# Optimization experiments

Hardware: AMD Instinct MI355X
Metric: run time of the kernel (lower is better)

Reference implementation:

```python
import jax, jax.numpy as jnp
import numpy as np

B, N, F, F1 = 1024, 75, 512, 256
NEG = -1.0e9
ALPHA = 0.2  # LeakyReLU slope


def setup_inputs() -> dict:
    key = jax.random.key(0)
    k1, k2, k3, k4 = jax.random.split(key, 4)
    X = jax.random.normal(k1, (B, N, F), dtype=jnp.float32)
    A = jax.random.randint(k2, (N, N), 0, 2, dtype=jnp.int32)  # binary adjacency
    W = jax.random.normal(k3, (F, F1), dtype=jnp.float32) * (1.0 / np.sqrt(F))
    a = jax.random.normal(k4, (2, F1, 1), dtype=jnp.float32) * (1.0 / np.sqrt(F1))
    return {"X": X, "A": A, "W": W, "a": a}


def reference(X, A, W, a):
    # Linear projection: [B, N, F1]
    h = jnp.einsum('bnf,fo->bno', X, W)
    # Additive attention logits
    att_self = jnp.einsum('bno,od->bnd', h, a[0])        # [B, N, 1]
    att_neigh = jnp.einsum('bno,od->bnd', h, a[1])       # [B, N, 1]
    e = att_self + jnp.swapaxes(att_neigh, 1, 2)         # [B, N, N]
    e = jax.nn.leaky_relu(e, ALPHA)
    # Adjacency mask: disallowed edges get large negative bias
    adj = A.astype(h.dtype)                               # [N, N]
    e = e + NEG * (1.0 - adj)[None, :, :]
    # Normalize over neighbors, aggregate
    alpha = jax.nn.softmax(e, axis=-1)                    # [B, N, N]
    out = jnp.einsum('bij,bjo->bio', alpha, h)            # [B, N, F1]
    return jnp.concatenate([out, h], axis=-1)             # [B, N, 2*F1]
```

## Files before the change

kernel.cpp:

```cpp
#include <hip/hip_runtime.h>
#include <hip/hip_bf16.h>
#include <math.h>

typedef __bf16 bf16_t;
typedef __bf16 bf16x4_t __attribute__((ext_vector_type(4)));
typedef __bf16 bf16x8 __attribute__((ext_vector_type(8)));
typedef float f32x4 __attribute__((ext_vector_type(4)));
typedef unsigned long long u64;

#define NB 1024
#define NN 75
#define KF 512
#define F1 256
#define HSTR 100
#define ASTR 100

__global__ __launch_bounds__(256) void wt_kernel(const float* __restrict__ W,
                                                 bf16_t* __restrict__ Wt) {
    __shared__ float tile[64][65];
    const int kb = blockIdx.x * 64;
    const int nb = blockIdx.y * 64;
    const int tc = threadIdx.x & 63;
    const int tr = threadIdx.x >> 6;
#pragma unroll
    for (int r = tr; r < 64; r += 4)
        tile[r][tc] = W[(size_t)(kb + r) * F1 + nb + tc];
    __syncthreads();
#pragma unroll
    for (int r = tr; r < 64; r += 4)
        Wt[(size_t)(nb + r) * KF + kb + tc] = (bf16_t)tile[tc][r];
}

__global__ __launch_bounds__(256) void gemm_kernel(const float* __restrict__ X,
                                                   const bf16_t* __restrict__ Wt,
                                                   float* __restrict__ out) {
    __shared__ __align__(16) bf16_t Xb[2 * 2048];

    const int t = threadIdx.x;
    const int w = t >> 6;
    const int l = t & 63;
    const int lc = l & 15;
    const int lr = l >> 4;
    const int m0 = blockIdx.x * 64;

    const int xrow  = ((t >> 6) << 4) + (t & 15);
    const int kpart = ((t >> 4) & 3) * 8;
    const float* xsrc = X + (size_t)(m0 + xrow) * KF + kpart;

    const bf16_t* wp0 = Wt + (size_t)(w * 64 + 0 * 16 + lc) * KF + lr * 8;
    const bf16_t* wp1 = Wt + (size_t)(w * 64 + 1 * 16 + lc) * KF + lr * 8;
    const bf16_t* wp2 = Wt + (size_t)(w * 64 + 2 * 16 + lc) * KF + lr * 8;
    const bf16_t* wp3 = Wt + (size_t)(w * 64 + 3 * 16 + lc) * KF + lr * 8;

    f32x4 acc[4][4];
#pragma unroll
    for (int i = 0; i < 4; ++i)
#pragma unroll
        for (int j = 0; j < 4; ++j) acc[i][j] = (f32x4){0.f, 0.f, 0.f, 0.f};

    float4 xa, xb;
    bf16x8 wA[4], wB[4];

#define WLOAD(WREG, KS)                                        \
    WREG[0] = *(const bf16x8*)(wp0 + (KS) * 32);               \
    WREG[1] = *(const bf16x8*)(wp1 + (KS) * 32);               \
    WREG[2] = *(const bf16x8*)(wp2 + (KS) * 32);               \
    WREG[3] = *(const bf16x8*)(wp3 + (KS) * 32);

#define GSTEP(KS, WREG)                                                        \
    {                                                                          \
        const bf16_t* Xc = Xb + ((KS) & 1) * 2048;                             \
        bf16x8 af[4];                                                          \
        _Pragma("unroll")                                                      \
        for (int mt = 0; mt < 4; ++mt)                                         \
            af[mt] = *(const bf16x8*)&Xc[(mt * 64 + l) * 8];                   \
        _Pragma("unroll")                                                      \
        for (int mt = 0; mt < 4; ++mt)                                         \
            _Pragma("unroll")                                                  \
            for (int ntl = 0; ntl < 4; ++ntl)                                  \
                acc[mt][ntl] = __builtin_amdgcn_mfma_f32_16x16x32_bf16(        \
                    af[mt], WREG[ntl], acc[mt][ntl], 0, 0, 0);                 \
        if ((KS) < 15) {                                                       \
            bf16x8 v;                                                          \
            v[0]=(bf16_t)xa.x; v[1]=(bf16_t)xa.y;                              \
            v[2]=(bf16_t)xa.z; v[3]=(bf16_t)xa.w;                              \
            v[4]=(bf16_t)xb.x; v[5]=(bf16_t)xb.y;                              \
            v[6]=(bf16_t)xb.z; v[7]=(bf16_t)xb.w;                              \
            *(bf16x8*)&Xb[(((KS) + 1) & 1) * 2048 + t * 8] = v;                \
            if ((KS) < 14) {                                                   \
                xa = *(const float4*)(xsrc + ((KS) + 2) * 32);                 \
                xb = *(const float4*)(xsrc + ((KS) + 2) * 32 + 4);             \
            }                                                                  \
        }                                                                      \
        __syncthreads();                                                       \
    }

    WLOAD(wA, 0);
    {
        xa = *(const float4*)xsrc;
        xb = *(const float4*)(xsrc + 4);
        bf16x8 v;
        v[0]=(bf16_t)xa.x; v[1]=(bf16_t)xa.y; v[2]=(bf16_t)xa.z; v[3]=(bf16_t)xa.w;
        v[4]=(bf16_t)xb.x; v[5]=(bf16_t)xb.y; v[6]=(bf16_t)xb.z; v[7]=(bf16_t)xb.w;
        *(bf16x8*)&Xb[t * 8] = v;
        xa = *(const float4*)(xsrc + 32);
        xb = *(const float4*)(xsrc + 36);
    }
    __syncthreads();

#pragma unroll
    for (int kp = 0; kp < 8; ++kp) {
        const int ks0 = kp * 2;
        const int ks1 = kp * 2 + 1;
        WLOAD(wB, ks1);
        GSTEP(ks0, wA);
        if (ks1 < 15) { WLOAD(wA, ks1 + 1); }
        GSTEP(ks1, wB);
    }
#undef GSTEP
#undef WLOAD

#pragma unroll
    for (int mt = 0; mt < 4; ++mt) {
#pragma unroll
        for (int ntl = 0; ntl < 4; ++ntl) {
            const int col = w * 64 + ntl * 16 + lc;
#pragma unroll
            for (int j = 0; j < 4; ++j) {
                const int row = m0 + mt * 16 + lr * 4 + j;
                out[(size_t)row * 512 + 256 + col] = acc[mt][ntl][j];
            }
        }
    }
}

__global__ __launch_bounds__(256) void pv_kernel(const int* __restrict__ Adj,
                                                 const float* __restrict__ avec,
                                                 float* __restrict__ out) {
    __shared__ __align__(16) bf16_t hT[256 * HSTR];
    __shared__ __align__(16) bf16_t alp[80 * ASTR];
    __shared__ float a0s[F1], a1s[F1];
    __shared__ float attp0[4][80], attp1[4][80];
    __shared__ float att0s[80], att1s[80], rsums[80];
    __shared__ u64 adjb[160];

    const int b = blockIdx.x;
    const int t = threadIdx.x;
    const int w = t >> 6;
    const int l = t & 63;
    const int lc = l & 15;
    const int lr = l >> 4;
    float* outb = out + (size_t)b * NN * 512;

    a0s[t] = avec[t];
    a1s[t] = avec[F1 + t];
    for (int i = w; i < NN; i += 4) {
        const int v0 = Adj[i * NN + l];
        const int v1 = (l < NN - 64) ? Adj[i * NN + 64 + l] : 0;
        const u64 b0 = __ballot(v0 != 0);
        const u64 b1 = __ballot(v1 != 0);
        if (l == 0) { adjb[i * 2] = b0; adjb[i * 2 + 1] = b1; }
    }
    {
        int* z = (int*)&hT[t * HSTR + 80];
#pragma unroll
        for (int k = 0; k < 8; ++k) z[k] = 0;
    }
    __syncthreads();

    const int c0 = w * 64 + lc * 4;
    const float4 a04 = *(const float4*)&a0s[c0];
    const float4 a14 = *(const float4*)&a1s[c0];
#pragma unroll
    for (int jp = 0; jp < 5; ++jp) {
        const int j0 = jp * 16 + lr * 4;
        float hr[4][4];
#pragma unroll
        for (int r = 0; r < 4; ++r) {
            if (j0 + r < NN) {
                const float4 v = *(const float4*)(outb + (size_t)(j0 + r) * 512 + 256 + c0);
                hr[r][0] = v.x; hr[r][1] = v.y; hr[r][2] = v.z; hr[r][3] = v.w;
            } else {
                hr[r][0] = hr[r][1] = hr[r][2] = hr[r][3] = 0.f;
            }
        }
        float p0[4], p1[4];
#pragma unroll
        for (int r = 0; r < 4; ++r) {
            p0[r] = hr[r][0] * a04.x + hr[r][1] * a04.y + hr[r][2] * a04.z + hr[r][3] * a04.w;
            p1[r] = hr[r][0] * a14.x + hr[r][1] * a14.y + hr[r][2] * a14.z + hr[r][3] * a14.w;
        }
#pragma unroll
        for (int off = 1; off < 16; off <<= 1) {
#pragma unroll
            for (int r = 0; r < 4; ++r) {
                p0[r] += __shfl_xor(p0[r], off);
                p1[r] += __shfl_xor(p1[r], off);
            }
        }
        if (lc == 0) {
#pragma unroll
            for (int r = 0; r < 4; ++r) {
                attp0[w][j0 + r] = p0[r];
                attp1[w][j0 + r] = p1[r];
            }
        }
#pragma unroll
        for (int cc = 0; cc < 4; ++cc) {
            bf16x4_t v;
            v[0] = (bf16_t)hr[0][cc]; v[1] = (bf16_t)hr[1][cc];
            v[2] = (bf16_t)hr[2][cc]; v[3] = (bf16_t)hr[3][cc];
            *(bf16x4_t*)&hT[(c0 + cc) * HSTR + j0] = v;
        }
    }
    __syncthreads();

    if (t < 80)
        att0s[t] = attp0[0][t] + attp0[1][t] + attp0[2][t] + attp0[3][t];
    else if (t < 160)
        att1s[t - 80] = attp1[0][t - 80] + attp1[1][t - 80] + attp1[2][t - 80] + attp1[3][t - 80];
    else if (t < 240) {
        const int r = t - 160;
        if (r < NN) {
            for (int c = NN; c < 96; ++c) alp[r * ASTR + c] = (bf16_t)0.f;
        } else {
            for (int c = 0; c < 96; ++c) alp[r * ASTR + c] = (bf16_t)0.f;
        }
    }
    __syncthreads();

    {
        const int gid = t >> 2;
        const int k4 = t & 3;
#pragma unroll
        for (int r = 0; r < 2; ++r) {
            const int i = r * 64 + gid;
            if (i < NN) {
                const float a0i = att0s[i];
                const u64 w0 = adjb[i * 2];
                const u64 w1 = adjb[i * 2 + 1];
                float e[19];
                float m = -3.0e38f;
#pragma unroll
                for (int jj = 0; jj < 19; ++jj) {
                    const int j = jj * 4 + k4;
                    float ev = -3.0e38f;
                    if (j < NN) {
                        float x = a0i + att1s[j];
                        x = x > 0.f ? x : 0.2f * x;
                        const u64 wj = (j < 64) ? w0 : w1;
                        const int bit = (int)((wj >> (j & 63)) & 1);
                        ev = bit ? x : x - 1.0e9f;
                    }
                    e[jj] = ev;
                    m = fmaxf(m, ev);
                }
                m = fmaxf(m, __shfl_xor(m, 1));
                m = fmaxf(m, __shfl_xor(m, 2));
                float s = 0.f;
#pragma unroll
                for (int jj = 0; jj < 19; ++jj) {
                    const int j = jj * 4 + k4;
                    if (j < NN) {
                        const float ex = __expf(e[jj] - m);
                        s += ex;
                        alp[i * ASTR + j] = (bf16_t)ex;
                    }
                }
                s += __shfl_xor(s, 1);
                s += __shfl_xor(s, 2);
                if (k4 == 0) rsums[i] = 1.f / s;
            }
        }
    }
    __syncthreads();

    f32x4 acc2[5][4];
#pragma unroll
    for (int i = 0; i < 5; ++i)
#pragma unroll
        for (int j = 0; j < 4; ++j) acc2[i][j] = (f32x4){0.f, 0.f, 0.f, 0.f};

#pragma unroll
    for (int ks = 0; ks < 3; ++ks) {
        bf16x8 bv[4];
#pragma unroll
        for (int ntl = 0; ntl < 4; ++ntl) {
            const bf16_t* q = &hT[(w * 64 + ntl * 16 + lc) * HSTR + ks * 32 + lr * 8];
            ((uint2*)&bv[ntl])[0] = *(const uint2*)q;
            ((uint2*)&bv[ntl])[1] = *(const uint2*)(q + 4);
        }
#pragma unroll
        for (int mt = 0; mt < 5; ++mt) {
            const bf16_t* ap = &alp[(mt * 16 + lc) * ASTR + ks * 32 + lr * 8];
            bf16x8 av;
            ((uint2*)&av)[0] = *(const uint2*)ap;
            ((uint2*)&av)[1] = *(const uint2*)(ap + 4);
#pragma unroll
            for (int ntl = 0; ntl < 4; ++ntl)
                acc2[mt][ntl] = __builtin_amdgcn_mfma_f32_16x16x32_bf16(av, bv[ntl], acc2[mt][ntl], 0, 0, 0);
        }
    }

#pragma unroll
    for (int mt = 0; mt < 5; ++mt) {
#pragma unroll
        for (int j = 0; j < 4; ++j) {
            const int row = mt * 16 + lr * 4 + j;
            if (row < NN) {
                const float rsv = rsums[row];
#pragma unroll
                for (int ntl = 0; ntl < 4; ++ntl) {
                    const int ch = w * 64 + ntl * 16 + lc;
                    outb[(size_t)row * 512 + ch] = acc2[mt][ntl][j] * rsv;
                }
            }
        }
    }
}

extern "C" void kernel_launch(void* const* d_in, const int* in_sizes, int n_in,
                              void* d_out, int out_size, void* d_ws, size_t ws_size,
                              hipStream_t stream) {
    const float* X = (const float*)d_in[0];
    const int*   A = (const int*)d_in[1];
    const float* W = (const float*)d_in[2];
    const float* a = (const float*)d_in[3];
    float* out = (float*)d_out;
    bf16_t* Wt = (bf16_t*)d_ws;

    wt_kernel<<<dim3(KF / 64, F1 / 64), 256, 0, stream>>>(W, Wt);
    gemm_kernel<<<(NB * NN) / 64, 256, 0, stream>>>(X, Wt, out);
    pv_kernel<<<NB, 256, 0, stream>>>(A, a, out);
}
```

Baseline: 141.0 us.

## Stage full X tile in shared memory upfront, drop per-step barriers

Replaces the double-buffered X staging, which refilled a small LDS buffer each k-step behind a barrier, with one upfront pass. That pass loads the block's whole 64x512 X tile, converts it to bf16 and stores it in 64 KB of shared memory, then synchronizes once. The MFMA loop then reads LDS without any further __syncthreads, removing 16 barriers per block. In exchange, the global loads no longer overlap with compute, and the much larger LDS footprint lowers how many blocks fit per CU.

```diff
diff --git a/kernel.cpp b/kernel.cpp
--- a/kernel.cpp
+++ b/kernel.cpp
@@ -34,7 +34,7 @@
 __global__ __launch_bounds__(256) void gemm_kernel(const float* __restrict__ X,
                                                    const bf16_t* __restrict__ Wt,
                                                    float* __restrict__ out) {
-    __shared__ __align__(16) bf16_t Xb[2 * 2048];
+    __shared__ __align__(16) bf16_t Xs[64 * 512];
 
     const int t = threadIdx.x;
     const int w = t >> 6;
@@ -43,70 +43,53 @@
     const int lr = l >> 4;
     const int m0 = blockIdx.x * 64;
 
-    const int xrow  = ((t >> 6) << 4) + (t & 15);
-    const int kpart = ((t >> 4) & 3) * 8;
-    const float* xsrc = X + (size_t)(m0 + xrow) * KF + kpart;
-
     const bf16_t* wp0 = Wt + (size_t)(w * 64 + 0 * 16 + lc) * KF + lr * 8;
     const bf16_t* wp1 = Wt + (size_t)(w * 64 + 1 * 16 + lc) * KF + lr * 8;
     const bf16_t* wp2 = Wt + (size_t)(w * 64 + 2 * 16 + lc) * KF + lr * 8;
     const bf16_t* wp3 = Wt + (size_t)(w * 64 + 3 * 16 + lc) * KF + lr * 8;
 
-    f32x4 acc[4][4];
-#pragma unroll
-    for (int i = 0; i < 4; ++i)
-#pragma unroll
-        for (int j = 0; j < 4; ++j) acc[i][j] = (f32x4){0.f, 0.f, 0.f, 0.f};
-
-    float4 xa, xb;
     bf16x8 wA[4], wB[4];
-
 #define WLOAD(WREG, KS)                                        \
     WREG[0] = *(const bf16x8*)(wp0 + (KS) * 32);               \
     WREG[1] = *(const bf16x8*)(wp1 + (KS) * 32);               \
     WREG[2] = *(const bf16x8*)(wp2 + (KS) * 32);               \
     WREG[3] = *(const bf16x8*)(wp3 + (KS) * 32);
 
+    WLOAD(wA, 0);
+
+    const int xrow  = ((t >> 6) << 4) + (t & 15);
+    const int kpart = ((t >> 4) & 3) * 8;
+    const float* xsrc = X + (size_t)(m0 + xrow) * KF + kpart;
+#pragma unroll
+    for (int q = 0; q < 16; ++q) {
+        const float4 xa = *(const float4*)(xsrc + q * 32);
+        const float4 xb = *(const float4*)(xsrc + q * 32 + 4);
+        bf16x8 v;
+        v[0]=(bf16_t)xa.x; v[1]=(bf16_t)xa.y; v[2]=(bf16_t)xa.z; v[3]=(bf16_t)xa.w;
+        v[4]=(bf16_t)xb.x; v[5]=(bf16_t)xb.y; v[6]=(bf16_t)xb.z; v[7]=(bf16_t)xb.w;
+        *(bf16x8*)&Xs[(q * 256 + t) * 8] = v;
+    }
+    __syncthreads();
+
+    f32x4 acc[4][4];
+#pragma unroll
+    for (int i = 0; i < 4; ++i)
+#pragma unroll
+        for (int j = 0; j < 4; ++j) acc[i][j] = (f32x4){0.f, 0.f, 0.f, 0.f};
+
 #define GSTEP(KS, WREG)                                                        \
     {                                                                          \
-        const bf16_t* Xc = Xb + ((KS) & 1) * 2048;                             \
         bf16x8 af[4];                                                          \
         _Pragma("unroll")                                                      \
         for (int mt = 0; mt < 4; ++mt)                                         \
-            af[mt] = *(const bf16x8*)&Xc[(mt * 64 + l) * 8];                   \
+            af[mt] = *(const bf16x8*)&Xs[((KS) * 256 + mt * 64 + l) * 8];      \
         _Pragma("unroll")                                                      \
         for (int mt = 0; mt < 4; ++mt)                                         \
             _Pragma("unroll")                                                  \
             for (int ntl = 0; ntl < 4; ++ntl)                                  \
                 acc[mt][ntl] = __builtin_amdgcn_mfma_f32_16x16x32_bf16(        \
                     af[mt], WREG[ntl], acc[mt][ntl], 0, 0, 0);                 \
-        if ((KS) < 15) {                                                       \
-            bf16x8 v;                                                          \
-            v[0]=(bf16_t)xa.x; v[1]=(bf16_t)xa.y;                              \
-            v[2]=(bf16_t)xa.z; v[3]=(bf16_t)xa.w;                              \
-            v[4]=(bf16_t)xb.x; v[5]=(bf16_t)xb.y;                              \
-            v[6]=(bf16_t)xb.z; v[7]=(bf16_t)xb.w;                              \
-            *(bf16x8*)&Xb[(((KS) + 1) & 1) * 2048 + t * 8] = v;                \
-            if ((KS) < 14) {                                                   \
-                xa = *(const float4*)(xsrc + ((KS) + 2) * 32);                 \
-                xb = *(const float4*)(xsrc + ((KS) + 2) * 32 + 4);             \
-            }                                                                  \
-        }                                                                      \
-        __syncthreads();                                                       \
-    }
-
-    WLOAD(wA, 0);
-    {
-        xa = *(const float4*)xsrc;
-        xb = *(const float4*)(xsrc + 4);
-        bf16x8 v;
-        v[0]=(bf16_t)xa.x; v[1]=(bf16_t)xa.y; v[2]=(bf16_t)xa.z; v[3]=(bf16_t)xa.w;
-        v[4]=(bf16_t)xb.x; v[5]=(bf16_t)xb.y; v[6]=(bf16_t)xb.z; v[7]=(bf16_t)xb.w;
-        *(bf16x8*)&Xb[t * 8] = v;
-        xa = *(const float4*)(xsrc + 32);
-        xb = *(const float4*)(xsrc + 36);
-    }
-    __syncthreads();
+    }
 
 #pragma unroll
     for (int kp = 0; kp < 8; ++kp) {
```

New measurement: 131.8 us. 1.07x faster.
